# Kernel tuning notes

Measured on AMD Instinct MI355X. Metric: run time of the kernel, lower is better.

Reference implementation:

```python
import jax, jax.numpy as jnp
import numpy as np

WH, WW = 7, 7
N = WH * WW
H = 16          # num_heads
D = 32          # head_dim
NW = 64         # num windows per image (mask.shape[0])


def _relative_position_index(wh, ww):
    coords = np.stack(np.meshgrid(np.arange(wh), np.arange(ww), indexing='ij'))  # (2, wh, ww)
    cf = coords.reshape(2, -1)                                                   # (2, N)
    rel = cf[:, :, None] - cf[:, None, :]                                        # (2, N, N)
    rel = rel.transpose(1, 2, 0).copy()
    rel[:, :, 0] += wh - 1
    rel[:, :, 1] += ww - 1
    rel[:, :, 0] *= 2 * ww - 1
    return rel.sum(-1)  # (N, N) int

REL_IDX = jnp.asarray(_relative_position_index(WH, WW))


def setup_inputs() -> dict:
    key = jax.random.key(0)
    ks = jax.random.split(key, 5)
    B_ = 2048
    dim = H * D
    x = jax.random.normal(ks[0], (B_, N, dim), dtype=jnp.float32)
    mask = jnp.zeros((NW, N, N), dtype=jnp.float32)
    rpb_table = jax.random.normal(ks[1], ((2 * WH - 1) * (2 * WW - 1), H), dtype=jnp.float32) * 0.02
    qkv_w = jax.random.normal(ks[2], (3 * dim, dim), dtype=jnp.float32) * (dim ** -0.5)
    qkv_b = jnp.zeros((3 * dim,), dtype=jnp.float32)
    proj_w = jax.random.normal(ks[3], (dim, dim), dtype=jnp.float32) * (dim ** -0.5)
    proj_b = jnp.zeros((dim,), dtype=jnp.float32)
    return {"x": x, "mask": mask, "rpb_table": rpb_table,
            "qkv_w": qkv_w, "qkv_b": qkv_b, "proj_w": proj_w, "proj_b": proj_b}


def reference(x, mask, rpb_table, qkv_w, qkv_b, proj_w, proj_b):
    B_, n, C = x.shape
    scale = D ** -0.5
    # qkv projection (torch Linear: x @ W^T + b)
    qkv = (x @ qkv_w.T + qkv_b).reshape(B_, n, 3, H, D)
    q = qkv[:, :, 0].transpose(0, 2, 1, 3) * scale  # (B_, H, N, D)
    k = qkv[:, :, 1].transpose(0, 2, 1, 3)
    v = qkv[:, :, 2].transpose(0, 2, 1, 3)
    attn = jnp.einsum('bhnd,bhmd->bhnm', q, k)      # (B_, H, N, N)
    # relative position bias: gather (N*N,) rows from table -> (N, N, H) -> (H, N, N)
    bias = rpb_table[REL_IDX.reshape(-1)].reshape(n, n, H).transpose(2, 0, 1)
    attn = attn + bias[None]
    # shifted-window mask add: (B, nW, H, N, N) + (1, nW, 1, N, N)
    nW = mask.shape[0]
    attn = attn.reshape(B_ // nW, nW, H, n, n) + mask[None, :, None]
    attn = attn.reshape(B_, H, n, n)
    attn = jax.nn.softmax(attn, axis=-1)
    out = jnp.einsum('bhnm,bhmd->bhnd', attn, v)    # (B_, H, N, D)
    out = out.transpose(0, 2, 1, 3).reshape(B_, n, H * D)
    return out @ proj_w.T + proj_b
```

## Files before the change

### kernel.cpp

```cpp
#include <hip/hip_runtime.h>

typedef _Float16 f16;
typedef _Float16 f16x8 __attribute__((ext_vector_type(8)));
typedef _Float16 f16x4 __attribute__((ext_vector_type(4)));
typedef __fp16 fp16x2 __attribute__((ext_vector_type(2)));
typedef float f32x4 __attribute__((ext_vector_type(4)));

#define NTOK 49
#define NH 16
#define HD 32
#define DIM 512
#define NWIN 64
#define NB 2048
#define MTOT (NB*NTOK)
#define SCALE 0.17677669529663687f
#define VTS 56

__device__ __forceinline__ void gload_lds16(const f16* g, f16* l) {
    __builtin_amdgcn_global_load_lds((const __attribute__((address_space(1))) void*)g,
                                     (__attribute__((address_space(3))) void*)l, 16, 0, 0);
}

__device__ __forceinline__ void cvt_body(const float* __restrict__ s, f16* __restrict__ d,
                                         int n4, int bid, int nb) {
    int i = bid * 256 + threadIdx.x;
    int st = nb * 256;
    for (; i < n4; i += st) {
        float4 v = ((const float4*)s)[i];
        f16x4 o = { (f16)v.x, (f16)v.y, (f16)v.z, (f16)v.w };
        *(f16x4*)(d + (size_t)i * 4) = o;
    }
}

__global__ __launch_bounds__(256) void cvt_f32_f16(const float* __restrict__ s,
                                                   f16* __restrict__ d, int n4) {
    cvt_body(s, d, n4, blockIdx.x, gridDim.x);
}

__global__ __launch_bounds__(256) void prep_kernel(const float* __restrict__ rpb,
                                                   const float* __restrict__ mask,
                                                   f16* __restrict__ comb2,
                                                   const float* __restrict__ qkvw,
                                                   f16* __restrict__ w16,
                                                   const float* __restrict__ projw,
                                                   f16* __restrict__ pw16) {
    const int bid = blockIdx.x;
    if (bid >= 16384) {
        if (bid < 16384 + 768) cvt_body(qkvw, w16, 1536 * 512 / 4, bid - 16384, 768);
        else                   cvt_body(projw, pw16, 512 * 512 / 4, bid - 16384 - 768, 256);
        return;
    }
    int idx = bid * 256 + threadIdx.x;
    int r4   = idx & 3;
    int tj   = (idx >> 2) & 3;
    int ti   = (idx >> 4) & 3;
    int lane = (idx >> 6) & 63;
    int wh   = idx >> 12;
    int h = wh & 15, w = wh >> 4;
    int g = lane >> 4, c16 = lane & 15;
    int k = ti * 16 + g * 4 + r4;
    int q = tj * 16 + c16;
    float v;
    if (k >= NTOK)      v = -30000.f;
    else if (q >= NTOK) v = 0.f;
    else {
        int rq = q / 7, cq = q - rq * 7;
        int rk = k / 7, ck = k - rk * 7;
        int rel = (rq - rk + 6) * 13 + (cq - ck + 6);
        v = rpb[rel * NH + h] + mask[(w * NTOK + q) * NTOK + k];
    }
    comb2[idx] = (f16)v;
}

#define WAIT_LGKM  asm volatile("s_waitcnt lgkmcnt(0)" ::: "memory")
#define WAIT_VM(N) asm volatile("s_waitcnt vmcnt(" #N ")" ::: "memory")

template<int MODE, int NT>
__global__ __launch_bounds__(512) void gemm_kernel(const f16* __restrict__ A,
                                                   const f16* __restrict__ Bw,
                                                   const float* __restrict__ bias,
                                                   f16* __restrict__ qo,
                                                   f16* __restrict__ ko,
                                                   f16* __restrict__ vto,
                                                   float* __restrict__ outp) {
    __shared__ __align__(16) f16 As[2][256][64];
    __shared__ __align__(16) f16 Bs[2][256][64];

    const int tid = threadIdx.x;
    const int lane = tid & 63;
    const int wv = tid >> 6;
    const int wm = wv >> 2, wn = wv & 3;
    const int g = lane >> 4, c16 = lane & 15;

    const int nblk = gridDim.x;
    const int f = blockIdx.x;
    const int work = (f & 7) * (nblk >> 3) + (f >> 3);
    const int m0 = (work / NT) * 256;
    const int n0 = (work % NT) * 256;

    const int srow = lane >> 3;
    const int schunk = (lane & 7) ^ srow;
    const f16* gA = A  + (size_t)(m0 + wv * 16 + srow) * DIM + schunk * 8;
    const f16* gB = Bw + (size_t)(n0 + wv * 16 + srow) * DIM + schunk * 8;

#define STAGE1(buf, kt, role) do {                                             \
    const f16* _s = (((role) < 2) ? gA : gB) + (size_t)(((role) & 1) * 128) * DIM + (kt) * 64; \
    f16* _d = ((role) < 2) ? &As[buf][((role) & 1) * 128 + wv * 16][0]         \
                           : &Bs[buf][((role) & 1) * 128 + wv * 16][0];        \
    gload_lds16(_s, _d);                                                       \
    gload_lds16(_s + (size_t)8 * DIM, _d + 8 * 64);                            \
} while (0)
#define STAGE_T(buf, kt) do { STAGE1(buf, kt, 0); STAGE1(buf, kt, 1);          \
                              STAGE1(buf, kt, 2); STAGE1(buf, kt, 3); } while (0)

#define READS(buf, kk, AF, BF) do {                                            \
    _Pragma("unroll") for (int _i = 0; _i < 8; ++_i)                           \
        (AF)[_i] = *(const f16x8*)&As[buf][wm * 128 + _i * 16 + c16][(((kk) * 4 + g) ^ (c16 & 7)) * 8]; \
    _Pragma("unroll") for (int _j = 0; _j < 4; ++_j)                           \
        (BF)[_j] = *(const f16x8*)&Bs[buf][wn * 64 + _j * 16 + c16][(((kk) * 4 + g) ^ (c16 & 7)) * 8]; \
} while (0)

#define MM(AF, BF) do {                                                        \
    __builtin_amdgcn_s_setprio(1);                                             \
    _Pragma("unroll") for (int _j = 0; _j < 4; ++_j)                           \
    _Pragma("unroll") for (int _i = 0; _i < 8; ++_i)                           \
        acc[_j][_i] = __builtin_amdgcn_mfma_f32_16x16x32_f16((BF)[_j], (AF)[_i], acc[_j][_i], 0, 0, 0); \
    __builtin_amdgcn_s_setprio(0);                                             \
} while (0)

    f32x4 acc[4][8];
#pragma unroll
    for (int j = 0; j < 4; ++j)
#pragma unroll
        for (int i = 0; i < 8; ++i)
            acc[j][i] = (f32x4){0.f, 0.f, 0.f, 0.f};

    f16x8 a0[8], b0[4], a1[8], b1[4];

    const int KT = DIM / 64;

    STAGE_T(0, 0);
    STAGE_T(1, 1);
    WAIT_VM(8);
    __builtin_amdgcn_s_barrier();
    READS(0, 0, a0, b0);

#pragma unroll
    for (int t = 0; t < KT; ++t) {
        const int b = t & 1, nb = b ^ 1;

        READS(b, 1, a1, b1);
        MM(a0, b0);
        WAIT_LGKM;
        __builtin_amdgcn_s_barrier();
        if (t + 2 < KT) STAGE_T(b, t + 2);
        if (t + 2 < KT) { WAIT_VM(8); }
        else if (t + 1 < KT) { WAIT_VM(0); }

        if (t + 1 < KT) READS(nb, 0, a0, b0);
        MM(a1, b1);
    }
#undef STAGE1
#undef STAGE_T
#undef READS
#undef MM

#pragma unroll
    for (int i = 0; i < 8; ++i) {
        const int m = m0 + wm * 128 + i * 16 + c16;
        int bb = 0, tk = 0;
        if (MODE == 0) { bb = m / NTOK; tk = m - bb * NTOK; }
#pragma unroll
        for (int j = 0; j < 4; ++j) {
            const int n = n0 + wn * 64 + j * 16 + g * 4;
            f32x4 v = acc[j][i];
            const f32x4 b4 = *(const f32x4*)&bias[n];
            v += b4;
            if (MODE == 0) {
                const int s = n >> 9;
                const int hh = (n >> 5) & 15;
                const int d0 = n & 31;
                const size_t bh = (size_t)(bb * NH + hh);
                if (s == 0) {
                    f16x4 o = { (f16)(v[0] * SCALE), (f16)(v[1] * SCALE),
                                (f16)(v[2] * SCALE), (f16)(v[3] * SCALE) };
                    *(f16x4*)(qo + (bh * NTOK + tk) * HD + d0) = o;
                } else if (s == 1) {
                    f16x4 o = { (f16)v[0], (f16)v[1], (f16)v[2], (f16)v[3] };
                    *(f16x4*)(ko + (bh * NTOK + tk) * HD + d0) = o;
                } else {
#pragma unroll
                    for (int r = 0; r < 4; ++r)
                        vto[(bh * HD + d0 + r) * VTS + tk] = (f16)v[r];
                }
            } else {
                float4 o = { v[0], v[1], v[2], v[3] };
                *(float4*)(outp + (size_t)m * DIM + n) = o;
            }
        }
    }
}

__global__ __launch_bounds__(256) void attn_kernel(const f16* __restrict__ qw,
                                                   const f16* __restrict__ kw,
                                                   const f16* __restrict__ vt,
                                                   const f16* __restrict__ comb2,
                                                   f16* __restrict__ aout) {
    __shared__ __align__(16) f16 Ps[4][64][72];

    const int wv = threadIdx.x >> 6;
    const int l = threadIdx.x & 63;
    const int f = blockIdx.x;
    const int work = (f & 7) * (gridDim.x >> 3) + (f >> 3);
    const int bid = work * 4 + wv;
    const int b = bid >> 4, h = bid & 15;
    const int w = b & (NWIN - 1);
    const int g = l >> 4, c16 = l & 15;
    const size_t qkbase = (size_t)bid * (NTOK * HD);
    const size_t vbase = (size_t)bid * (HD * VTS);

    const f16x8 z8 = {};

    f16x8 qf[4], kf[4];
#pragma unroll
    for (int t = 0; t < 4; ++t) {
        int row = t * 16 + c16;
        f16x8 q = z8, k = z8;
        if (row < NTOK) {
            q = *(const f16x8*)(qw + qkbase + row * HD + g * 8);
            k = *(const f16x8*)(kw + qkbase + row * HD + g * 8);
        }
        qf[t] = q; kf[t] = k;
    }

    const f16* cb = comb2 + (((size_t)(w * NH + h) * 64 + l) << 6);
    f16x8 cbv[8];
#pragma unroll
    for (int k = 0; k < 8; ++k) cbv[k] = *(const f16x8*)(cb + k * 8);
    f32x4 St[4][4];
#pragma unroll
    for (int i = 0; i < 4; ++i)
#pragma unroll
        for (int j = 0; j < 4; ++j) {
            const int e = i * 16 + j * 4;
#pragma unroll
            for (int r = 0; r < 4; ++r)
                St[i][j][r] = (float)cbv[(e + r) >> 3][(e + r) & 7];
        }
#pragma unroll
    for (int i = 0; i < 4; ++i)
#pragma unroll
        for (int j = 0; j < 4; ++j)
            St[i][j] = __builtin_amdgcn_mfma_f32_16x16x32_f16(kf[i], qf[j], St[i][j], 0, 0, 0);

    float inv[4];
#pragma unroll
    for (int j = 0; j < 4; ++j) {
        float m = St[0][j][0];
#pragma unroll
        for (int i = 0; i < 4; ++i)
#pragma unroll
            for (int r = 0; r < 4; ++r) m = fmaxf(m, St[i][j][r]);
        m = fmaxf(m, __shfl_xor(m, 16, 64));
        m = fmaxf(m, __shfl_xor(m, 32, 64));
        float s = 0.f;
#pragma unroll
        for (int i = 0; i < 4; ++i)
#pragma unroll
            for (int r = 0; r < 4; ++r) {
                float p = __expf(St[i][j][r] - m);
                St[i][j][r] = p;
                s += p;
            }
        s += __shfl_xor(s, 16, 64);
        s += __shfl_xor(s, 32, 64);
        inv[j] = 1.f / s;
    }

#pragma unroll
    for (int j = 0; j < 4; ++j) {
        const int q = j * 16 + c16;
#pragma unroll
        for (int i = 0; i < 4; ++i) {
            fp16x2 u0 = __builtin_amdgcn_cvt_pkrtz(St[i][j][0], St[i][j][1]);
            fp16x2 u1 = __builtin_amdgcn_cvt_pkrtz(St[i][j][2], St[i][j][3]);
            *(fp16x2*)&Ps[wv][q][i * 16 + 4 * g]     = u0;
            *(fp16x2*)&Ps[wv][q][i * 16 + 4 * g + 2] = u1;
        }
    }
    WAIT_LGKM;

    f32x4 O2[2][4];
    const f32x4 zf = (f32x4){0.f, 0.f, 0.f, 0.f};
#pragma unroll
    for (int td = 0; td < 2; ++td)
#pragma unroll
        for (int ti = 0; ti < 4; ++ti) O2[td][ti] = zf;
#pragma unroll
    for (int c = 0; c < 2; ++c) {
        f16x8 pf[4], vf[2];
#pragma unroll
        for (int ti = 0; ti < 4; ++ti)
            pf[ti] = *(const f16x8*)&Ps[wv][ti * 16 + c16][c * 32 + g * 8];
        int tcol = c * 32 + g * 8;
#pragma unroll
        for (int td = 0; td < 2; ++td) {
            f16x8 vv = z8;
            if (tcol < VTS)
                vv = *(const f16x8*)(vt + vbase + (size_t)(td * 16 + c16) * VTS + tcol);
            vf[td] = vv;
        }
#pragma unroll
        for (int td = 0; td < 2; ++td)
#pragma unroll
            for (int ti = 0; ti < 4; ++ti)
                O2[td][ti] = __builtin_amdgcn_mfma_f32_16x16x32_f16(vf[td], pf[ti], O2[td][ti], 0, 0, 0);
    }

#pragma unroll
    for (int ti = 0; ti < 4; ++ti) {
        int tok = ti * 16 + c16;
        if (tok < NTOK) {
            size_t ob = ((size_t)(b * NTOK + tok)) * DIM + h * HD;
#pragma unroll
            for (int td = 0; td < 2; ++td) {
                f32x4 v = O2[td][ti];
                float iv = inv[ti];
                f16x4 o = { (f16)(v[0] * iv), (f16)(v[1] * iv),
                            (f16)(v[2] * iv), (f16)(v[3] * iv) };
                *(f16x4*)(aout + ob + td * 16 + g * 4) = o;
            }
        }
    }
}

extern "C" void kernel_launch(void* const* d_in, const int* in_sizes, int n_in,
                              void* d_out, int out_size, void* d_ws, size_t ws_size,
                              hipStream_t stream) {
    const float* x      = (const float*)d_in[0];
    const float* mask   = (const float*)d_in[1];
    const float* rpb    = (const float*)d_in[2];
    const float* qkv_w  = (const float*)d_in[3];
    const float* qkv_b  = (const float*)d_in[4];
    const float* proj_w = (const float*)d_in[5];
    const float* proj_b = (const float*)d_in[6];
    float* out = (float*)d_out;

    char* ws = (char*)d_ws;
    size_t o = 0;
    f16* x16   = (f16*)(ws + o); o += (size_t)MTOT * DIM * 2;
    f16* w16   = (f16*)(ws + o); o += (size_t)1536 * 512 * 2;
    f16* pw16  = (f16*)(ws + o); o += (size_t)512 * 512 * 2;
    f16* qws   = (f16*)(ws + o); o += (size_t)NB * NH * NTOK * HD * 2;
    f16* kws   = (f16*)(ws + o); o += (size_t)NB * NH * NTOK * HD * 2;
    f16* vtws  = (f16*)(ws + o); o += (size_t)NB * NH * HD * VTS * 2;
    f16* cb2   = (f16*)(ws + o);
    f16* aout = x16;

    cvt_f32_f16<<<dim3(2048), dim3(256), 0, stream>>>(x, x16, MTOT * DIM / 4);

    prep_kernel<<<dim3(16384 + 768 + 256), dim3(256), 0, stream>>>(
        rpb, mask, cb2, qkv_w, w16, proj_w, pw16);

    gemm_kernel<0, 6><<<dim3((MTOT / 256) * 6), dim3(512), 0, stream>>>(
        x16, w16, qkv_b, qws, kws, vtws, nullptr);

    attn_kernel<<<dim3(NB * NH / 4), dim3(256), 0, stream>>>(qws, kws, vtws, cb2, aout);

    gemm_kernel<1, 2><<<dim3((MTOT / 256) * 2), dim3(512), 0, stream>>>(
        aout, pw16, proj_b, nullptr, nullptr, nullptr, out);
}
```

Measured before the change: 542.6 us.

## Use 128x128 triple-buffered GEMM for projection and fold x conversion into prep

```diff
diff --git a/kernel.cpp b/kernel.cpp
--- a/kernel.cpp
+++ b/kernel.cpp
@@ -32,22 +32,20 @@
     }
 }
 
-__global__ __launch_bounds__(256) void cvt_f32_f16(const float* __restrict__ s,
-                                                   f16* __restrict__ d, int n4) {
-    cvt_body(s, d, n4, blockIdx.x, gridDim.x);
-}
-
 __global__ __launch_bounds__(256) void prep_kernel(const float* __restrict__ rpb,
                                                    const float* __restrict__ mask,
                                                    f16* __restrict__ comb2,
                                                    const float* __restrict__ qkvw,
                                                    f16* __restrict__ w16,
                                                    const float* __restrict__ projw,
-                                                   f16* __restrict__ pw16) {
+                                                   f16* __restrict__ pw16,
+                                                   const float* __restrict__ x,
+                                                   f16* __restrict__ x16) {
     const int bid = blockIdx.x;
     if (bid >= 16384) {
-        if (bid < 16384 + 768) cvt_body(qkvw, w16, 1536 * 512 / 4, bid - 16384, 768);
-        else                   cvt_body(projw, pw16, 512 * 512 / 4, bid - 16384 - 768, 256);
+        if (bid < 16384 + 2048)      cvt_body(x, x16, MTOT * DIM / 4, bid - 16384, 2048);
+        else if (bid < 16384 + 2816) cvt_body(qkvw, w16, 1536 * 512 / 4, bid - 16384 - 2048, 768);
+        else                         cvt_body(projw, pw16, 512 * 512 / 4, bid - 16384 - 2816, 256);
         return;
     }
     int idx = bid * 256 + threadIdx.x;
@@ -75,14 +73,13 @@
 #define WAIT_LGKM  asm volatile("s_waitcnt lgkmcnt(0)" ::: "memory")
 #define WAIT_VM(N) asm volatile("s_waitcnt vmcnt(" #N ")" ::: "memory")
 
-template<int MODE, int NT>
-__global__ __launch_bounds__(512) void gemm_kernel(const f16* __restrict__ A,
-                                                   const f16* __restrict__ Bw,
-                                                   const float* __restrict__ bias,
-                                                   f16* __restrict__ qo,
-                                                   f16* __restrict__ ko,
-                                                   f16* __restrict__ vto,
-                                                   float* __restrict__ outp) {
+template<int NT>
+__global__ __launch_bounds__(512) void gemm256(const f16* __restrict__ A,
+                                               const f16* __restrict__ Bw,
+                                               const float* __restrict__ bias,
+                                               f16* __restrict__ qo,
+                                               f16* __restrict__ ko,
+                                               f16* __restrict__ vto) {
     __shared__ __align__(16) f16 As[2][256][64];
     __shared__ __align__(16) f16 Bs[2][256][64];
 
@@ -168,35 +165,119 @@
 #pragma unroll
     for (int i = 0; i < 8; ++i) {
         const int m = m0 + wm * 128 + i * 16 + c16;
-        int bb = 0, tk = 0;
-        if (MODE == 0) { bb = m / NTOK; tk = m - bb * NTOK; }
+        const int bb = m / NTOK, tk = m - (m / NTOK) * NTOK;
 #pragma unroll
         for (int j = 0; j < 4; ++j) {
             const int n = n0 + wn * 64 + j * 16 + g * 4;
             f32x4 v = acc[j][i];
             const f32x4 b4 = *(const f32x4*)&bias[n];
             v += b4;
-            if (MODE == 0) {
-                const int s = n >> 9;
-                const int hh = (n >> 5) & 15;
-                const int d0 = n & 31;
-                const size_t bh = (size_t)(bb * NH + hh);
-                if (s == 0) {
-                    f16x4 o = { (f16)(v[0] * SCALE), (f16)(v[1] * SCALE),
-                                (f16)(v[2] * SCALE), (f16)(v[3] * SCALE) };
-                    *(f16x4*)(qo + (bh * NTOK + tk) * HD + d0) = o;
-                } else if (s == 1) {
-                    f16x4 o = { (f16)v[0], (f16)v[1], (f16)v[2], (f16)v[3] };
-                    *(f16x4*)(ko + (bh * NTOK + tk) * HD + d0) = o;
-                } else {
-#pragma unroll
-                    for (int r = 0; r < 4; ++r)
-                        vto[(bh * HD + d0 + r) * VTS + tk] = (f16)v[r];
-                }
+            const int s = n >> 9;
+            const int hh = (n >> 5) & 15;
+            const int d0 = n & 31;
+            const size_t bh = (size_t)(bb * NH + hh);
+            if (s == 0) {
+                f16x4 o = { (f16)(v[0] * SCALE), (f16)(v[1] * SCALE),
+                            (f16)(v[2] * SCALE), (f16)(v[3] * SCALE) };
+                *(f16x4*)(qo + (bh * NTOK + tk) * HD + d0) = o;
+            } else if (s == 1) {
+                f16x4 o = { (f16)v[0], (f16)v[1], (f16)v[2], (f16)v[3] };
+                *(f16x4*)(ko + (bh * NTOK + tk) * HD + d0) = o;
             } else {
-                float4 o = { v[0], v[1], v[2], v[3] };
-                *(float4*)(outp + (size_t)m * DIM + n) = o;
+#pragma unroll
+                for (int r = 0; r < 4; ++r)
+                    vto[(bh * HD + d0 + r) * VTS + tk] = (f16)v[r];
             }
+        }
+    }
+}
+
+__global__ __launch_bounds__(256, 3) void gemm128(const f16* __restrict__ A,
+                                                  const f16* __restrict__ Bw,
+                                                  const float* __restrict__ bias,
+                                                  float* __restrict__ outp) {
+    __shared__ __align__(16) f16 As[3][128][32];
+    __shared__ __align__(16) f16 Bs[3][128][32];
+
+    const int NT = 4;
+    const int tid = threadIdx.x;
+    const int lane = tid & 63;
+    const int wv = tid >> 6;
+    const int wr = wv >> 1, wc = wv & 1;
+    const int g = lane >> 4, c16 = lane & 15;
+    const int rsw = (c16 >> 1) & 3;
+
+    const int nblk = gridDim.x;
+    const int f = blockIdx.x;
+    const int work = (f & 7) * (nblk >> 3) + (f >> 3);
+    const int m0 = (work / NT) * 128;
+    const int n0 = (work % NT) * 128;
+
+    const int srow = lane >> 2;
+    const int schunk = (lane & 3) ^ ((srow >> 1) & 3);
+    const f16* gA = A  + (size_t)(m0 + wv * 32 + srow) * DIM + schunk * 8;
+    const f16* gB = Bw + (size_t)(n0 + wv * 32 + srow) * DIM + schunk * 8;
+
+#define STAGE6(buf, t) do { \
+    gload_lds16(gA + (t) * 32,                     &As[buf][wv * 32][0]);      \
+    gload_lds16(gA + (size_t)16 * DIM + (t) * 32,  &As[buf][wv * 32 + 16][0]); \
+    gload_lds16(gB + (t) * 32,                     &Bs[buf][wv * 32][0]);      \
+    gload_lds16(gB + (size_t)16 * DIM + (t) * 32,  &Bs[buf][wv * 32 + 16][0]); \
+} while (0)
+
+    f32x4 acc[4][4];
+#pragma unroll
+    for (int j = 0; j < 4; ++j)
+#pragma unroll
+        for (int i = 0; i < 4; ++i)
+            acc[j][i] = (f32x4){0.f, 0.f, 0.f, 0.f};
+
+    STAGE6(0, 0);
+    STAGE6(1, 1);
+    WAIT_VM(4);
+    __builtin_amdgcn_s_barrier();
+
+    const int KS = DIM / 32;
+#pragma unroll
+    for (int t = 0; t < KS; ++t) {
+        const int cb = t % 3;
+        if (t + 2 < KS) STAGE6((t + 2) % 3, t + 2);
+        f16x8 af[4], bf[4];
+#pragma unroll
+        for (int i = 0; i < 4; ++i)
+            af[i] = *(const f16x8*)&As[cb][wr * 64 + i * 16 + c16][(g ^ rsw) * 8];
+#pragma unroll
+        for (int j = 0; j < 4; ++j)
+            bf[j] = *(const f16x8*)&Bs[cb][wc * 64 + j * 16 + c16][(g ^ rsw) * 8];
+        __builtin_amdgcn_s_setprio(1);
+#pragma unroll
+        for (int j = 0; j < 4; ++j)
+#pragma unroll
+            for (int i = 0; i < 4; ++i)
+                acc[j][i] = __builtin_amdgcn_mfma_f32_16x16x32_f16(bf[j], af[i], acc[j][i], 0, 0, 0);
+        __builtin_amdgcn_s_setprio(0);
+        WAIT_LGKM;
+        __builtin_amdgcn_sched_barrier(0);
+        if (t + 2 < KS) {
+            WAIT_VM(4);
+        } else if (t + 1 < KS) {
+            WAIT_VM(0);
+        }
+        if (t + 1 < KS) __builtin_amdgcn_s_barrier();
+    }
+#undef STAGE6
+
+#pragma unroll
+    for (int i = 0; i < 4; ++i) {
+        const int m = m0 + wr * 64 + i * 16 + c16;
+#pragma unroll
+        for (int j = 0; j < 4; ++j) {
+            const int n = n0 + wc * 64 + j * 16 + g * 4;
+            f32x4 v = acc[j][i];
+            const f32x4 b4 = *(const f32x4*)&bias[n];
+            v += b4;
+            float4 o = { v[0], v[1], v[2], v[3] };
+            *(float4*)(outp + (size_t)m * DIM + n) = o;
         }
     }
 }
@@ -357,16 +438,14 @@
     f16* cb2   = (f16*)(ws + o);
     f16* aout = x16;
 
-    cvt_f32_f16<<<dim3(2048), dim3(256), 0, stream>>>(x, x16, MTOT * DIM / 4);
-
-    prep_kernel<<<dim3(16384 + 768 + 256), dim3(256), 0, stream>>>(
-        rpb, mask, cb2, qkv_w, w16, proj_w, pw16);
-
-    gemm_kernel<0, 6><<<dim3((MTOT / 256) * 6), dim3(512), 0, stream>>>(
-        x16, w16, qkv_b, qws, kws, vtws, nullptr);
+    prep_kernel<<<dim3(16384 + 2048 + 768 + 256), dim3(256), 0, stream>>>(
+        rpb, mask, cb2, qkv_w, w16, proj_w, pw16, x, x16);
+
+    gemm256<6><<<dim3((MTOT / 256) * 6), dim3(512), 0, stream>>>(
+        x16, w16, qkv_b, qws, kws, vtws);
 
     attn_kernel<<<dim3(NB * NH / 4), dim3(256), 0, stream>>>(qws, kws, vtws, cb2, aout);
 
-    gemm_kernel<1, 2><<<dim3((MTOT / 256) * 2), dim3(512), 0, stream>>>(
-        aout, pw16, proj_b, nullptr, nullptr, nullptr, out);
-}
+    gemm128<<<dim3((MTOT / 128) * 4), dim3(256), 0, stream>>>(
+        aout, pw16, proj_b, out);
+}
```

Result: faster. 529.7 us (median of 2 runs) (-2.4%).
